# Performance work log

Hardware: AMD Instinct MI355X
Metric: run time of the kernel (lower is better)

## Reference

```python
import jax, jax.numpy as jnp
import numpy as np

K = 8          # max_output_degree (complete 8-ary tree)
DEPTH = 7      # number of levels
LEVEL_OFFS = [(K**l - 1) // (K - 1) for l in range(DEPTH + 1)]  # [0,1,9,73,...]
N = LEVEL_OFFS[DEPTH]  # 299593 nodes
V, X, H, O = 32000, 128, 128, 128


def setup_inputs() -> dict:
    key = jax.random.key(0)
    ks = jax.random.split(key, 7)
    x = jax.random.randint(ks[0], (N,), 0, V, dtype=jnp.int32)
    mask = jnp.ones((N,), dtype=jnp.int32)
    # children of node i are K*i+1 .. K*i+K; out-of-range -> sentinel N (zero pad row)
    ch = np.arange(N, dtype=np.int64)[:, None] * K + 1 + np.arange(K, dtype=np.int64)[None, :]
    children = jnp.asarray(np.where(ch < N, ch, N).astype(np.int32))
    s = 0.02
    emb = jax.random.normal(ks[1], (V, X), dtype=jnp.float32) * s
    W_in = jax.random.normal(ks[2], (X, H), dtype=jnp.float32) * s
    b_in = jnp.zeros((H,), dtype=jnp.float32)
    U = jax.random.normal(ks[3], (H, H), dtype=jnp.float32) * s
    W_out = jax.random.normal(ks[4], (H, O), dtype=jnp.float32) * s
    b_out = jnp.zeros((O,), dtype=jnp.float32)
    return {"x": x, "mask": mask, "children": children, "emb": emb,
            "W_in": W_in, "b_in": b_in, "U": U, "W_out": W_out, "b_out": b_out}


def reference(x, mask, children, emb, W_in, b_in, U, b_out=None, W_out=None, **_):
    # keyword-safe wrapper not used; real signature below
    raise NotImplementedError


def reference(x, mask, children, emb, W_in, b_in, U, W_out, b_out):
    mf = mask.astype(jnp.float32)[:, None]                 # [N,1]
    embeds = emb[x * mask]                                 # [N,X] input_module(x*mask)
    h_input = (embeds @ W_in + b_in) * mf                  # [N,H] W_in(embeds)*mask
    h = jnp.zeros((N + 1, h_input.shape[1]), dtype=h_input.dtype)  # row N = zero pad
    # bottom-up topological propagation, level by level
    for l in range(DEPTH - 1, -1, -1):
        s, e = LEVEL_OFFS[l], LEVEL_OFFS[l + 1]
        if l == DEPTH - 1:
            # leaves: no children messages
            h_new = jnp.tanh(h_input[s:e])
        else:
            h_ch = h[children[s:e]]                        # [n_l,K,H] gather child states
            agg = h_ch.sum(axis=1) @ U                     # SumChild aggregator + linear
            h_new = jnp.tanh(h_input[s:e] + agg)           # apply_node_func
        h = h.at[s:e].set(h_new)
    out = h[:N] @ W_out + b_out                            # output_module
    return out
```

## Files before the change

### kernel.cpp

```cpp
#include <hip/hip_runtime.h>
#include <hip/hip_bf16.h>


typedef __bf16 bf16x8 __attribute__((ext_vector_type(8)));
typedef float f32x4 __attribute__((ext_vector_type(4)));
typedef float f32x2 __attribute__((ext_vector_type(2)));
typedef unsigned short ushort8 __attribute__((ext_vector_type(8)));
typedef unsigned int uint2v __attribute__((ext_vector_type(2)));

#define NNODES 299593
#define NPAR   37449

static __device__ __forceinline__ unsigned short f2bf(float f) {
  union { float f; unsigned int u; } v; v.f = f;
  unsigned int u = v.u;
  u += 0x7fff + ((u >> 16) & 1);
  return (unsigned short)(u >> 16);
}

static __device__ __forceinline__ unsigned int pk2bf(float a, float b) {
#if __has_builtin(__builtin_amdgcn_cvt_pk_bf16_f32)
  typedef __bf16 bf16x2 __attribute__((ext_vector_type(2)));
  union { bf16x2 v; unsigned int u; } c;
  c.v = __builtin_amdgcn_cvt_pk_bf16_f32(a, b);
  return c.u;
#else
  return (unsigned int)f2bf(a) | ((unsigned int)f2bf(b) << 16);
#endif
}

static __device__ __forceinline__ float fast_tanh(float x) {
  float y = x * 2.885390081777927f;
#if __has_builtin(__builtin_amdgcn_exp2f)
  float e = __builtin_amdgcn_exp2f(y);
#else
  float e = __builtin_exp2f(y);
#endif
#if __has_builtin(__builtin_amdgcn_rcpf)
  float r = __builtin_amdgcn_rcpf(e + 1.0f);
#else
  float r = 1.0f / (e + 1.0f);
#endif
  return __builtin_fmaf(-2.0f, r, 1.0f);
}

__global__ __launch_bounds__(256) void prep_kernel(
    const float* __restrict__ W_in, const float* __restrict__ U,
    const float* __restrict__ W_out, const float* __restrict__ emb,
    unsigned short* __restrict__ w_sw, unsigned short* __restrict__ emb_bf) {
  int t = blockIdx.x * 256 + threadIdx.x;
  if (blockIdx.x < 192) {
    int f = t;
    int m = f >> 14;
    int r = f & 16383;
    int j = r & 7;
    int lane = (r >> 3) & 63;
    int nt = (r >> 9) & 7;
    int kt = (r >> 12) & 3;
    int k = kt * 32 + ((lane >> 4) * 8) + j;
    int n = nt * 16 + (lane & 15);
    const float* W = (m == 0) ? W_in : (m == 1) ? U : W_out;
    w_sw[f] = f2bf(W[k * 128 + n]);
  } else {
    size_t i = (size_t)(t - 49152) * 8;
    f32x4 v0 = *(const f32x4*)(emb + i);
    f32x4 v1 = *(const f32x4*)(emb + i + 4);
    union { ushort8 s; unsigned int u[4]; } w;
    w.u[0] = pk2bf(v0[0], v0[1]);
    w.u[1] = pk2bf(v0[2], v0[3]);
    w.u[2] = pk2bf(v1[0], v1[1]);
    w.u[3] = pk2bf(v1[2], v1[3]);
    *(ushort8*)(emb_bf + i) = w.s;
  }
}

static __device__ __forceinline__ bf16x8 ldz(const unsigned short* p, int nz) {
  union { bf16x8 b; unsigned int u[4]; } v;
  v.b = *(const bf16x8*)p;
  if (!nz) { v.u[0] = 0; v.u[1] = 0; v.u[2] = 0; v.u[3] = 0; }
  return v.b;
}

static __device__ __forceinline__ void mfma_row8(f32x4 acc[8], bf16x8 a,
    const unsigned short* __restrict__ bkt, int lane) {
#pragma unroll
  for (int nt = 0; nt < 8; ++nt) {
    bf16x8 b = *(const bf16x8*)(bkt + nt * 512 + lane * 8);
    acc[nt] = __builtin_amdgcn_mfma_f32_16x16x32_bf16(a, b, acc[nt], 0, 0, 0);
  }
}

template <bool LEAF>
static __device__ __forceinline__ void tile_body(
    const int* __restrict__ x, const int* __restrict__ mask,
    const unsigned short* __restrict__ emb_bf,
    const float* __restrict__ b_in, const float* __restrict__ b_out,
    const unsigned short* __restrict__ w_sw,
    unsigned short* __restrict__ cs, float* __restrict__ out,
    int e, int row0, unsigned short (*Abuf)[136], int tid) {
  const int lane = tid & 63;
  const int wave = tid >> 6;
  const int coll = lane & 15;
  const int quad = lane >> 4;

  const int garow = row0 + wave * 16 + coll;
  const int valid = garow < e;
  const int m = valid ? mask[garow] : 0;
  const int idx = valid ? x[garow] * m : 0;

  const unsigned short* arow = emb_bf + (size_t)idx * 128 + quad * 8;
  bf16x8 ea0 = ldz(arow, m);
  bf16x8 ea1 = ldz(arow + 32, m);
  bf16x8 ea2 = ldz(arow + 64, m);
  bf16x8 ea3 = ldz(arow + 96, m);
  bf16x8 ca0, ca1, ca2, ca3;
  if (!LEAF) {
    const unsigned short* crow = cs + (size_t)garow * 128 + quad * 8;
    ca0 = ldz(crow, valid);
    ca1 = ldz(crow + 32, valid);
    ca2 = ldz(crow + 64, valid);
    ca3 = ldz(crow + 96, valid);
  }

  f32x4 acc[8];
#pragma unroll
  for (int nt = 0; nt < 8; ++nt) acc[nt] = (f32x4){0.f, 0.f, 0.f, 0.f};

  mfma_row8(acc, ea0, w_sw, lane);
  mfma_row8(acc, ea1, w_sw + 4096, lane);
  mfma_row8(acc, ea2, w_sw + 8192, lane);
  mfma_row8(acc, ea3, w_sw + 12288, lane);

  if (!LEAF) {
    mfma_row8(acc, ca0, w_sw + 16384, lane);
    mfma_row8(acc, ca1, w_sw + 20480, lane);
    mfma_row8(acc, ca2, w_sw + 24576, lane);
    mfma_row8(acc, ca3, w_sw + 28672, lane);
  }

  float binv[8];
#pragma unroll
  for (int nt = 0; nt < 8; ++nt) binv[nt] = b_in[nt * 16 + coll];
#pragma unroll
  for (int r2 = 0; r2 < 4; ++r2) {
    const int rowl = wave * 16 + quad * 4 + r2;
    const int grow = row0 + rowl;
    const float mval = (grow < e) ? (float)mask[grow] : 0.f;
#pragma unroll
    for (int nt = 0; nt < 8; ++nt) {
      float t = acc[nt][r2] + mval * binv[nt];
      Abuf[rowl][nt * 16 + coll] = f2bf(fast_tanh(t));
    }
  }
  __builtin_amdgcn_wave_barrier();

  if (row0 > 0) {
    const int j = lane >> 5;
    const int c4 = (lane & 31) * 4;
    const int childrow0 = row0 + (wave * 2 + j) * 8;
    if (childrow0 < e) {
      const int lr0 = wave * 16 + j * 8;
      f32x2 sA = {0.f, 0.f}, sB = {0.f, 0.f};
#pragma unroll
      for (int r = 0; r < 8; ++r) {
        const unsigned int* pr =
            (const unsigned int*)&Abuf[lr0 + r][c4];
        unsigned int u0 = pr[0], u1 = pr[1];
        union { unsigned int u; float f; } l0, h0, l1, h1;
        l0.u = u0 << 16; h0.u = u0 & 0xffff0000u;
        l1.u = u1 << 16; h1.u = u1 & 0xffff0000u;
        sA += (f32x2){l0.f, h0.f};
        sB += (f32x2){l1.f, h1.f};
      }
      uint2v w;
      w.x = pk2bf(sA[0], sA[1]);
      w.y = pk2bf(sB[0], sB[1]);
      const int p = ((row0 - 1) >> 3) + wave * 2 + j;
      *(uint2v*)(cs + (size_t)p * 128 + c4) = w;
    }
  }

  f32x4 oacc[8];
#pragma unroll
  for (int nt = 0; nt < 8; ++nt) oacc[nt] = (f32x4){0.f, 0.f, 0.f, 0.f};
  const unsigned short* ab = &Abuf[wave * 16][0] + coll * 136 + quad * 8;
#pragma unroll
  for (int kt = 0; kt < 4; ++kt) {
    bf16x8 a = *(const bf16x8*)(ab + kt * 32);
    mfma_row8(oacc, a, w_sw + 32768 + kt * 4096, lane);
  }

  float boutv[8];
#pragma unroll
  for (int nt = 0; nt < 8; ++nt) boutv[nt] = b_out[nt * 16 + coll];
#pragma unroll
  for (int r2 = 0; r2 < 4; ++r2) {
    const int rowl = wave * 16 + quad * 4 + r2;
    const int grow = row0 + rowl;
    if (grow < e) {
#pragma unroll
      for (int nt = 0; nt < 8; ++nt)
        out[(size_t)grow * 128 + nt * 16 + coll] = oacc[nt][r2] + boutv[nt];
    }
  }
}

template <bool LEAF>
__global__ __launch_bounds__(256) void level_kernel(
    const int* __restrict__ x, const int* __restrict__ mask,
    const unsigned short* __restrict__ emb_bf, const float* __restrict__ b_in,
    const float* __restrict__ b_out, const unsigned short* __restrict__ w_sw,
    unsigned short* __restrict__ cs, float* __restrict__ out, int s, int e) {
  __shared__ __align__(16) unsigned short Abuf[64][136];
  tile_body<LEAF>(x, mask, emb_bf, b_in, b_out, w_sw, cs, out, e,
                  s + blockIdx.x * 64, Abuf, threadIdx.x);
}

__global__ __launch_bounds__(256) void tail_kernel(
    const int* __restrict__ x, const int* __restrict__ mask,
    const unsigned short* __restrict__ emb_bf, const float* __restrict__ b_in,
    const float* __restrict__ b_out, const unsigned short* __restrict__ w_sw,
    unsigned short* __restrict__ cs, float* __restrict__ out) {
  __shared__ __align__(16) unsigned short Abuf[64][136];
  tile_body<false>(x, mask, emb_bf, b_in, b_out, w_sw, cs, out, 73, 9, Abuf,
                   threadIdx.x);
  __syncthreads();
  tile_body<false>(x, mask, emb_bf, b_in, b_out, w_sw, cs, out, 9, 1, Abuf,
                   threadIdx.x);
  __syncthreads();
  tile_body<false>(x, mask, emb_bf, b_in, b_out, w_sw, cs, out, 1, 0, Abuf,
                   threadIdx.x);
}

extern "C" void kernel_launch(void* const* d_in, const int* in_sizes, int n_in,
                              void* d_out, int out_size, void* d_ws,
                              size_t ws_size, hipStream_t stream) {
  const int* x = (const int*)d_in[0];
  const int* mask = (const int*)d_in[1];
  const float* emb = (const float*)d_in[3];
  const float* W_in = (const float*)d_in[4];
  const float* b_in = (const float*)d_in[5];
  const float* U = (const float*)d_in[6];
  const float* W_out = (const float*)d_in[7];
  const float* b_out = (const float*)d_in[8];
  float* out = (float*)d_out;

  unsigned short* emb_bf = (unsigned short*)d_ws;
  unsigned short* cs = emb_bf + (size_t)32000 * 128;
  unsigned short* w_sw = cs + (size_t)NPAR * 128;

  prep_kernel<<<2192, 256, 0, stream>>>(W_in, U, W_out, emb, w_sw, emb_bf);

  level_kernel<true><<<4096, 256, 0, stream>>>(x, mask, emb_bf, b_in, b_out,
                                               w_sw, cs, out, 37449, 299593);
  level_kernel<false><<<512, 256, 0, stream>>>(x, mask, emb_bf, b_in, b_out,
                                               w_sw, cs, out, 4681, 37449);
  level_kernel<false><<<64, 256, 0, stream>>>(x, mask, emb_bf, b_in, b_out,
                                              w_sw, cs, out, 585, 4681);
  level_kernel<false><<<8, 256, 0, stream>>>(x, mask, emb_bf, b_in, b_out,
                                             w_sw, cs, out, 73, 585);
  tail_kernel<<<1, 256, 0, stream>>>(x, mask, emb_bf, b_in, b_out, w_sw, cs,
                                     out);
}
```

Measured before the change: 278.0 us.

## Process two 16-row sub-tiles per wave to reuse each weight fragment load

Each wave now handles 32 rows instead of 16, so every block covers 128 nodes. Each B-fragment load from the swizzled weights feeds two MFMAs (one per sub-tile), which halves weight traffic per row. Grid sizes are halved and the LDS tile doubles to 128 rows. The cost is roughly double the accumulator registers, which may lower occupancy, and fewer blocks on the smaller levels.

```diff
diff --git a/kernel.cpp b/kernel.cpp
--- a/kernel.cpp
+++ b/kernel.cpp
@@ -81,12 +81,14 @@
   return v.b;
 }
 
-static __device__ __forceinline__ void mfma_row8(f32x4 acc[8], bf16x8 a,
-    const unsigned short* __restrict__ bkt, int lane) {
+static __device__ __forceinline__ void mfma8x2(
+    f32x4 (&acc0)[8], f32x4 (&acc1)[8], bf16x8 a0, bf16x8 a1,
+    const unsigned short* __restrict__ bp) {
 #pragma unroll
   for (int nt = 0; nt < 8; ++nt) {
-    bf16x8 b = *(const bf16x8*)(bkt + nt * 512 + lane * 8);
-    acc[nt] = __builtin_amdgcn_mfma_f32_16x16x32_bf16(a, b, acc[nt], 0, 0, 0);
+    bf16x8 b = *(const bf16x8*)(bp + nt * 512);
+    acc0[nt] = __builtin_amdgcn_mfma_f32_16x16x32_bf16(a0, b, acc0[nt], 0, 0, 0);
+    acc1[nt] = __builtin_amdgcn_mfma_f32_16x16x32_bf16(a1, b, acc1[nt], 0, 0, 0);
   }
 }
 
@@ -103,106 +105,133 @@
   const int coll = lane & 15;
   const int quad = lane >> 4;
 
-  const int garow = row0 + wave * 16 + coll;
-  const int valid = garow < e;
-  const int m = valid ? mask[garow] : 0;
-  const int idx = valid ? x[garow] * m : 0;
-
-  const unsigned short* arow = emb_bf + (size_t)idx * 128 + quad * 8;
-  bf16x8 ea0 = ldz(arow, m);
-  bf16x8 ea1 = ldz(arow + 32, m);
-  bf16x8 ea2 = ldz(arow + 64, m);
-  bf16x8 ea3 = ldz(arow + 96, m);
-  bf16x8 ca0, ca1, ca2, ca3;
+  const int ga0 = row0 + wave * 32 + coll;
+  const int ga1 = ga0 + 16;
+  const int v0 = ga0 < e;
+  const int v1 = ga1 < e;
+  const int m0 = v0 ? mask[ga0] : 0;
+  const int m1 = v1 ? mask[ga1] : 0;
+  const int i0 = v0 ? x[ga0] * m0 : 0;
+  const int i1 = v1 ? x[ga1] * m1 : 0;
+
+  const unsigned short* a0p = emb_bf + (size_t)i0 * 128 + quad * 8;
+  const unsigned short* a1p = emb_bf + (size_t)i1 * 128 + quad * 8;
+  bf16x8 e00 = ldz(a0p, m0),      e10 = ldz(a1p, m1);
+  bf16x8 e01 = ldz(a0p + 32, m0), e11 = ldz(a1p + 32, m1);
+  bf16x8 e02 = ldz(a0p + 64, m0), e12 = ldz(a1p + 64, m1);
+  bf16x8 e03 = ldz(a0p + 96, m0), e13 = ldz(a1p + 96, m1);
+
+  const unsigned short* bl = w_sw + lane * 8;
+
+  f32x4 acc0[8], acc1[8];
+#pragma unroll
+  for (int nt = 0; nt < 8; ++nt) {
+    acc0[nt] = (f32x4){0.f, 0.f, 0.f, 0.f};
+    acc1[nt] = (f32x4){0.f, 0.f, 0.f, 0.f};
+  }
+
+  mfma8x2(acc0, acc1, e00, e10, bl);
+  mfma8x2(acc0, acc1, e01, e11, bl + 4096);
+  mfma8x2(acc0, acc1, e02, e12, bl + 8192);
+  mfma8x2(acc0, acc1, e03, e13, bl + 12288);
+
   if (!LEAF) {
-    const unsigned short* crow = cs + (size_t)garow * 128 + quad * 8;
-    ca0 = ldz(crow, valid);
-    ca1 = ldz(crow + 32, valid);
-    ca2 = ldz(crow + 64, valid);
-    ca3 = ldz(crow + 96, valid);
-  }
-
-  f32x4 acc[8];
-#pragma unroll
-  for (int nt = 0; nt < 8; ++nt) acc[nt] = (f32x4){0.f, 0.f, 0.f, 0.f};
-
-  mfma_row8(acc, ea0, w_sw, lane);
-  mfma_row8(acc, ea1, w_sw + 4096, lane);
-  mfma_row8(acc, ea2, w_sw + 8192, lane);
-  mfma_row8(acc, ea3, w_sw + 12288, lane);
-
-  if (!LEAF) {
-    mfma_row8(acc, ca0, w_sw + 16384, lane);
-    mfma_row8(acc, ca1, w_sw + 20480, lane);
-    mfma_row8(acc, ca2, w_sw + 24576, lane);
-    mfma_row8(acc, ca3, w_sw + 28672, lane);
+    const unsigned short* c0p = cs + (size_t)ga0 * 128 + quad * 8;
+    const unsigned short* c1p = cs + (size_t)ga1 * 128 + quad * 8;
+    bf16x8 c00 = ldz(c0p, v0),      c10 = ldz(c1p, v1);
+    bf16x8 c01 = ldz(c0p + 32, v0), c11 = ldz(c1p + 32, v1);
+    bf16x8 c02 = ldz(c0p + 64, v0), c12 = ldz(c1p + 64, v1);
+    bf16x8 c03 = ldz(c0p + 96, v0), c13 = ldz(c1p + 96, v1);
+    mfma8x2(acc0, acc1, c00, c10, bl + 16384);
+    mfma8x2(acc0, acc1, c01, c11, bl + 20480);
+    mfma8x2(acc0, acc1, c02, c12, bl + 24576);
+    mfma8x2(acc0, acc1, c03, c13, bl + 28672);
   }
 
   float binv[8];
 #pragma unroll
   for (int nt = 0; nt < 8; ++nt) binv[nt] = b_in[nt * 16 + coll];
-#pragma unroll
-  for (int r2 = 0; r2 < 4; ++r2) {
-    const int rowl = wave * 16 + quad * 4 + r2;
-    const int grow = row0 + rowl;
-    const float mval = (grow < e) ? (float)mask[grow] : 0.f;
-#pragma unroll
-    for (int nt = 0; nt < 8; ++nt) {
-      float t = acc[nt][r2] + mval * binv[nt];
-      Abuf[rowl][nt * 16 + coll] = f2bf(fast_tanh(t));
+
+  auto epi = [&](f32x4 (&ac)[8], int sub) {
+#pragma unroll
+    for (int r2 = 0; r2 < 4; ++r2) {
+      const int rowl = wave * 32 + sub * 16 + quad * 4 + r2;
+      const int grow = row0 + rowl;
+      const float mval = (grow < e) ? (float)mask[grow] : 0.f;
+#pragma unroll
+      for (int nt = 0; nt < 8; ++nt) {
+        float t = ac[nt][r2] + mval * binv[nt];
+        Abuf[rowl][nt * 16 + coll] = f2bf(fast_tanh(t));
+      }
     }
-  }
+  };
+  epi(acc0, 0);
+  epi(acc1, 1);
   __builtin_amdgcn_wave_barrier();
 
   if (row0 > 0) {
     const int j = lane >> 5;
     const int c4 = (lane & 31) * 4;
-    const int childrow0 = row0 + (wave * 2 + j) * 8;
-    if (childrow0 < e) {
-      const int lr0 = wave * 16 + j * 8;
-      f32x2 sA = {0.f, 0.f}, sB = {0.f, 0.f};
-#pragma unroll
-      for (int r = 0; r < 8; ++r) {
-        const unsigned int* pr =
-            (const unsigned int*)&Abuf[lr0 + r][c4];
-        unsigned int u0 = pr[0], u1 = pr[1];
-        union { unsigned int u; float f; } l0, h0, l1, h1;
-        l0.u = u0 << 16; h0.u = u0 & 0xffff0000u;
-        l1.u = u1 << 16; h1.u = u1 & 0xffff0000u;
-        sA += (f32x2){l0.f, h0.f};
-        sB += (f32x2){l1.f, h1.f};
+#pragma unroll
+    for (int sub = 0; sub < 2; ++sub) {
+      const int pidx = wave * 4 + sub * 2 + j;
+      const int childrow0 = row0 + pidx * 8;
+      if (childrow0 < e) {
+        const int lr0 = wave * 32 + sub * 16 + j * 8;
+        f32x2 sA = {0.f, 0.f}, sB = {0.f, 0.f};
+#pragma unroll
+        for (int r = 0; r < 8; ++r) {
+          const unsigned int* pr =
+              (const unsigned int*)&Abuf[lr0 + r][c4];
+          unsigned int u0 = pr[0], u1 = pr[1];
+          union { unsigned int u; float f; } l0, h0, l1, h1;
+          l0.u = u0 << 16; h0.u = u0 & 0xffff0000u;
+          l1.u = u1 << 16; h1.u = u1 & 0xffff0000u;
+          sA += (f32x2){l0.f, h0.f};
+          sB += (f32x2){l1.f, h1.f};
+        }
+        uint2v w;
+        w.x = pk2bf(sA[0], sA[1]);
+        w.y = pk2bf(sB[0], sB[1]);
+        const int p = ((row0 - 1) >> 3) + pidx;
+        *(uint2v*)(cs + (size_t)p * 128 + c4) = w;
       }
-      uint2v w;
-      w.x = pk2bf(sA[0], sA[1]);
-      w.y = pk2bf(sB[0], sB[1]);
-      const int p = ((row0 - 1) >> 3) + wave * 2 + j;
-      *(uint2v*)(cs + (size_t)p * 128 + c4) = w;
     }
   }
 
-  f32x4 oacc[8];
-#pragma unroll
-  for (int nt = 0; nt < 8; ++nt) oacc[nt] = (f32x4){0.f, 0.f, 0.f, 0.f};
-  const unsigned short* ab = &Abuf[wave * 16][0] + coll * 136 + quad * 8;
+  f32x4 o0[8], o1[8];
+#pragma unroll
+  for (int nt = 0; nt < 8; ++nt) {
+    o0[nt] = (f32x4){0.f, 0.f, 0.f, 0.f};
+    o1[nt] = (f32x4){0.f, 0.f, 0.f, 0.f};
+  }
+  const unsigned short* ab0 = &Abuf[wave * 32][0] + coll * 136 + quad * 8;
+  const unsigned short* ab1 = ab0 + 16 * 136;
 #pragma unroll
   for (int kt = 0; kt < 4; ++kt) {
-    bf16x8 a = *(const bf16x8*)(ab + kt * 32);
-    mfma_row8(oacc, a, w_sw + 32768 + kt * 4096, lane);
+    bf16x8 a0 = *(const bf16x8*)(ab0 + kt * 32);
+    bf16x8 a1 = *(const bf16x8*)(ab1 + kt * 32);
+    mfma8x2(o0, o1, a0, a1, bl + 32768 + kt * 4096);
   }
 
   float boutv[8];
 #pragma unroll
   for (int nt = 0; nt < 8; ++nt) boutv[nt] = b_out[nt * 16 + coll];
-#pragma unroll
-  for (int r2 = 0; r2 < 4; ++r2) {
-    const int rowl = wave * 16 + quad * 4 + r2;
-    const int grow = row0 + rowl;
-    if (grow < e) {
-#pragma unroll
-      for (int nt = 0; nt < 8; ++nt)
-        out[(size_t)grow * 128 + nt * 16 + coll] = oacc[nt][r2] + boutv[nt];
+
+  auto st = [&](f32x4 (&oc)[8], int sub) {
+#pragma unroll
+    for (int r2 = 0; r2 < 4; ++r2) {
+      const int rowl = wave * 32 + sub * 16 + quad * 4 + r2;
+      const int grow = row0 + rowl;
+      if (grow < e) {
+#pragma unroll
+        for (int nt = 0; nt < 8; ++nt)
+          out[(size_t)grow * 128 + nt * 16 + coll] = oc[nt][r2] + boutv[nt];
+      }
     }
-  }
+  };
+  st(o0, 0);
+  st(o1, 1);
 }
 
 template <bool LEAF>
@@ -211,9 +240,9 @@
     const unsigned short* __restrict__ emb_bf, const float* __restrict__ b_in,
     const float* __restrict__ b_out, const unsigned short* __restrict__ w_sw,
     unsigned short* __restrict__ cs, float* __restrict__ out, int s, int e) {
-  __shared__ __align__(16) unsigned short Abuf[64][136];
+  __shared__ __align__(16) unsigned short Abuf[128][136];
   tile_body<LEAF>(x, mask, emb_bf, b_in, b_out, w_sw, cs, out, e,
-                  s + blockIdx.x * 64, Abuf, threadIdx.x);
+                  s + blockIdx.x * 128, Abuf, threadIdx.x);
 }
 
 __global__ __launch_bounds__(256) void tail_kernel(
@@ -221,7 +250,7 @@
     const unsigned short* __restrict__ emb_bf, const float* __restrict__ b_in,
     const float* __restrict__ b_out, const unsigned short* __restrict__ w_sw,
     unsigned short* __restrict__ cs, float* __restrict__ out) {
-  __shared__ __align__(16) unsigned short Abuf[64][136];
+  __shared__ __align__(16) unsigned short Abuf[128][136];
   tile_body<false>(x, mask, emb_bf, b_in, b_out, w_sw, cs, out, 73, 9, Abuf,
                    threadIdx.x);
   __syncthreads();
@@ -251,13 +280,13 @@
 
   prep_kernel<<<2192, 256, 0, stream>>>(W_in, U, W_out, emb, w_sw, emb_bf);
 
-  level_kernel<true><<<4096, 256, 0, stream>>>(x, mask, emb_bf, b_in, b_out,
+  level_kernel<true><<<2048, 256, 0, stream>>>(x, mask, emb_bf, b_in, b_out,
                                                w_sw, cs, out, 37449, 299593);
-  level_kernel<false><<<512, 256, 0, stream>>>(x, mask, emb_bf, b_in, b_out,
+  level_kernel<false><<<256, 256, 0, stream>>>(x, mask, emb_bf, b_in, b_out,
                                                w_sw, cs, out, 4681, 37449);
-  level_kernel<false><<<64, 256, 0, stream>>>(x, mask, emb_bf, b_in, b_out,
+  level_kernel<false><<<32, 256, 0, stream>>>(x, mask, emb_bf, b_in, b_out,
                                               w_sw, cs, out, 585, 4681);
-  level_kernel<false><<<8, 256, 0, stream>>>(x, mask, emb_bf, b_in, b_out,
+  level_kernel<false><<<4, 256, 0, stream>>>(x, mask, emb_bf, b_in, b_out,
                                              w_sw, cs, out, 73, 585);
   tail_kernel<<<1, 256, 0, stream>>>(x, mask, emb_bf, b_in, b_out, w_sw, cs,
                                      out);
```

Result: slower. 323.5 us (+16.3%).

## Fuse upper tree levels into one persistent kernel with grid barriers

Applied to the files above, without the earlier changes.

Replaces the four upper-level launches and the tail kernel with a single 512-block kernel that walks levels 5 down to 0, separated by atomic-counter grid barriers. Child-sum buffers are read and written through agent-scope relaxed atomics so data is visible across blocks without a kernel boundary. Output stores become nontemporal. This removes several launch gaps in exchange for spin-wait barriers, which rely on all 512 blocks being co-resident and on barrier counters reset in the prep kernel.

```diff
diff --git a/kernel.cpp b/kernel.cpp
--- a/kernel.cpp
+++ b/kernel.cpp
@@ -10,6 +10,7 @@
 
 #define NNODES 299593
 #define NPAR   37449
+#define NBLK_UPPER 512
 
 static __device__ __forceinline__ unsigned short f2bf(float f) {
   union { float f; unsigned int u; } v; v.f = f;
@@ -47,8 +48,12 @@
 __global__ __launch_bounds__(256) void prep_kernel(
     const float* __restrict__ W_in, const float* __restrict__ U,
     const float* __restrict__ W_out, const float* __restrict__ emb,
-    unsigned short* __restrict__ w_sw, unsigned short* __restrict__ emb_bf) {
+    unsigned short* __restrict__ w_sw, unsigned short* __restrict__ emb_bf,
+    unsigned int* __restrict__ bar) {
   int t = blockIdx.x * 256 + threadIdx.x;
+  if (t < 8)
+    __hip_atomic_store(bar + t, 0u, __ATOMIC_RELAXED,
+                       __HIP_MEMORY_SCOPE_AGENT);
   if (blockIdx.x < 192) {
     int f = t;
     int m = f >> 14;
@@ -81,6 +86,18 @@
   return v.b;
 }
 
+static __device__ __forceinline__ bf16x8 ldz_agent(const unsigned short* p,
+                                                   int nz) {
+  union { bf16x8 b; unsigned int u[4]; } v;
+  const unsigned int* q = (const unsigned int*)p;
+  v.u[0] = __hip_atomic_load(q + 0, __ATOMIC_RELAXED, __HIP_MEMORY_SCOPE_AGENT);
+  v.u[1] = __hip_atomic_load(q + 1, __ATOMIC_RELAXED, __HIP_MEMORY_SCOPE_AGENT);
+  v.u[2] = __hip_atomic_load(q + 2, __ATOMIC_RELAXED, __HIP_MEMORY_SCOPE_AGENT);
+  v.u[3] = __hip_atomic_load(q + 3, __ATOMIC_RELAXED, __HIP_MEMORY_SCOPE_AGENT);
+  if (!nz) { v.u[0] = 0; v.u[1] = 0; v.u[2] = 0; v.u[3] = 0; }
+  return v.b;
+}
+
 static __device__ __forceinline__ void mfma_row8(f32x4 acc[8], bf16x8 a,
     const unsigned short* __restrict__ bkt, int lane) {
 #pragma unroll
@@ -90,7 +107,7 @@
   }
 }
 
-template <bool LEAF>
+template <bool LEAF, bool CS_LD_AGENT, bool CS_ST_AGENT>
 static __device__ __forceinline__ void tile_body(
     const int* __restrict__ x, const int* __restrict__ mask,
     const unsigned short* __restrict__ emb_bf,
@@ -116,10 +133,17 @@
   bf16x8 ca0, ca1, ca2, ca3;
   if (!LEAF) {
     const unsigned short* crow = cs + (size_t)garow * 128 + quad * 8;
-    ca0 = ldz(crow, valid);
-    ca1 = ldz(crow + 32, valid);
-    ca2 = ldz(crow + 64, valid);
-    ca3 = ldz(crow + 96, valid);
+    if constexpr (CS_LD_AGENT) {
+      ca0 = ldz_agent(crow, valid);
+      ca1 = ldz_agent(crow + 32, valid);
+      ca2 = ldz_agent(crow + 64, valid);
+      ca3 = ldz_agent(crow + 96, valid);
+    } else {
+      ca0 = ldz(crow, valid);
+      ca1 = ldz(crow + 32, valid);
+      ca2 = ldz(crow + 64, valid);
+      ca3 = ldz(crow + 96, valid);
+    }
   }
 
   f32x4 acc[8];
@@ -172,11 +196,18 @@
         sA += (f32x2){l0.f, h0.f};
         sB += (f32x2){l1.f, h1.f};
       }
-      uint2v w;
-      w.x = pk2bf(sA[0], sA[1]);
-      w.y = pk2bf(sB[0], sB[1]);
       const int p = ((row0 - 1) >> 3) + wave * 2 + j;
-      *(uint2v*)(cs + (size_t)p * 128 + c4) = w;
+      unsigned int wx = pk2bf(sA[0], sA[1]);
+      unsigned int wy = pk2bf(sB[0], sB[1]);
+      if constexpr (CS_ST_AGENT) {
+        unsigned int* q = (unsigned int*)(cs + (size_t)p * 128 + c4);
+        __hip_atomic_store(q, wx, __ATOMIC_RELAXED, __HIP_MEMORY_SCOPE_AGENT);
+        __hip_atomic_store(q + 1, wy, __ATOMIC_RELAXED,
+                           __HIP_MEMORY_SCOPE_AGENT);
+      } else {
+        uint2v w; w.x = wx; w.y = wy;
+        *(uint2v*)(cs + (size_t)p * 128 + c4) = w;
+      }
     }
   }
 
@@ -200,36 +231,68 @@
     if (grow < e) {
 #pragma unroll
       for (int nt = 0; nt < 8; ++nt)
-        out[(size_t)grow * 128 + nt * 16 + coll] = oacc[nt][r2] + boutv[nt];
+        __builtin_nontemporal_store(oacc[nt][r2] + boutv[nt],
+                                    &out[(size_t)grow * 128 + nt * 16 + coll]);
     }
   }
 }
 
-template <bool LEAF>
-__global__ __launch_bounds__(256) void level_kernel(
-    const int* __restrict__ x, const int* __restrict__ mask,
-    const unsigned short* __restrict__ emb_bf, const float* __restrict__ b_in,
-    const float* __restrict__ b_out, const unsigned short* __restrict__ w_sw,
-    unsigned short* __restrict__ cs, float* __restrict__ out, int s, int e) {
-  __shared__ __align__(16) unsigned short Abuf[64][136];
-  tile_body<LEAF>(x, mask, emb_bf, b_in, b_out, w_sw, cs, out, e,
-                  s + blockIdx.x * 64, Abuf, threadIdx.x);
-}
-
-__global__ __launch_bounds__(256) void tail_kernel(
+static __device__ __forceinline__ void grid_barrier(unsigned int* ctr,
+                                                    int tid) {
+  __syncthreads();
+  if (tid == 0) {
+    __hip_atomic_fetch_add(ctr, 1u, __ATOMIC_ACQ_REL,
+                           __HIP_MEMORY_SCOPE_AGENT);
+    while (__hip_atomic_load(ctr, __ATOMIC_ACQUIRE,
+                             __HIP_MEMORY_SCOPE_AGENT) < (unsigned)NBLK_UPPER)
+      __builtin_amdgcn_s_sleep(4);
+  }
+  __syncthreads();
+}
+
+__global__ __launch_bounds__(256) void leaf_kernel(
     const int* __restrict__ x, const int* __restrict__ mask,
     const unsigned short* __restrict__ emb_bf, const float* __restrict__ b_in,
     const float* __restrict__ b_out, const unsigned short* __restrict__ w_sw,
     unsigned short* __restrict__ cs, float* __restrict__ out) {
   __shared__ __align__(16) unsigned short Abuf[64][136];
-  tile_body<false>(x, mask, emb_bf, b_in, b_out, w_sw, cs, out, 73, 9, Abuf,
-                   threadIdx.x);
-  __syncthreads();
-  tile_body<false>(x, mask, emb_bf, b_in, b_out, w_sw, cs, out, 9, 1, Abuf,
-                   threadIdx.x);
-  __syncthreads();
-  tile_body<false>(x, mask, emb_bf, b_in, b_out, w_sw, cs, out, 1, 0, Abuf,
-                   threadIdx.x);
+  tile_body<true, false, false>(x, mask, emb_bf, b_in, b_out, w_sw, cs, out,
+                                299593, 37449 + blockIdx.x * 64, Abuf,
+                                threadIdx.x);
+}
+
+__global__ __launch_bounds__(256, 4) void upper_kernel(
+    const int* __restrict__ x, const int* __restrict__ mask,
+    const unsigned short* __restrict__ emb_bf, const float* __restrict__ b_in,
+    const float* __restrict__ b_out, const unsigned short* __restrict__ w_sw,
+    unsigned short* __restrict__ cs, float* __restrict__ out,
+    unsigned int* __restrict__ bar) {
+  __shared__ __align__(16) unsigned short Abuf[64][136];
+  const int bid = blockIdx.x;
+  const int tid = threadIdx.x;
+
+  tile_body<false, true, true>(x, mask, emb_bf, b_in, b_out, w_sw, cs, out,
+                               37449, 4681 + bid * 64, Abuf, tid);
+  grid_barrier(bar + 0, tid);
+  if (bid < 64)
+    tile_body<false, true, true>(x, mask, emb_bf, b_in, b_out, w_sw, cs, out,
+                                 4681, 585 + bid * 64, Abuf, tid);
+  grid_barrier(bar + 1, tid);
+  if (bid < 8)
+    tile_body<false, true, true>(x, mask, emb_bf, b_in, b_out, w_sw, cs, out,
+                                 585, 73 + bid * 64, Abuf, tid);
+  grid_barrier(bar + 2, tid);
+  if (bid == 0)
+    tile_body<false, true, true>(x, mask, emb_bf, b_in, b_out, w_sw, cs, out,
+                                 73, 9, Abuf, tid);
+  grid_barrier(bar + 3, tid);
+  if (bid == 0)
+    tile_body<false, true, true>(x, mask, emb_bf, b_in, b_out, w_sw, cs, out,
+                                 9, 1, Abuf, tid);
+  grid_barrier(bar + 4, tid);
+  if (bid == 0)
+    tile_body<false, true, true>(x, mask, emb_bf, b_in, b_out, w_sw, cs, out,
+                                 1, 0, Abuf, tid);
 }
 
 extern "C" void kernel_launch(void* const* d_in, const int* in_sizes, int n_in,
@@ -248,17 +311,14 @@
   unsigned short* emb_bf = (unsigned short*)d_ws;
   unsigned short* cs = emb_bf + (size_t)32000 * 128;
   unsigned short* w_sw = cs + (size_t)NPAR * 128;
-
-  prep_kernel<<<2192, 256, 0, stream>>>(W_in, U, W_out, emb, w_sw, emb_bf);
-
-  level_kernel<true><<<4096, 256, 0, stream>>>(x, mask, emb_bf, b_in, b_out,
-                                               w_sw, cs, out, 37449, 299593);
-  level_kernel<false><<<512, 256, 0, stream>>>(x, mask, emb_bf, b_in, b_out,
-                                               w_sw, cs, out, 4681, 37449);
-  level_kernel<false><<<64, 256, 0, stream>>>(x, mask, emb_bf, b_in, b_out,
-                                              w_sw, cs, out, 585, 4681);
-  level_kernel<false><<<8, 256, 0, stream>>>(x, mask, emb_bf, b_in, b_out,
-                                             w_sw, cs, out, 73, 585);
-  tail_kernel<<<1, 256, 0, stream>>>(x, mask, emb_bf, b_in, b_out, w_sw, cs,
-                                     out);
-}
+  unsigned int* bar = (unsigned int*)(w_sw + 49152);
+
+  prep_kernel<<<2192, 256, 0, stream>>>(W_in, U, W_out, emb, w_sw, emb_bf,
+                                        bar);
+
+  leaf_kernel<<<4096, 256, 0, stream>>>(x, mask, emb_bf, b_in, b_out, w_sw,
+                                        cs, out);
+
+  upper_kernel<<<NBLK_UPPER, 256, 0, stream>>>(x, mask, emb_bf, b_in, b_out,
+                                               w_sw, cs, out, bar);
+}
```

New measurement: 1.045 ms. +275.7%, slower.
